# Kernel tuning notes

Hardware: AMD Instinct MI355X
Metric: run time of the kernel (lower is better)

The kernel has to match this reference:

```python
import jax, jax.numpy as jnp
import numpy as np

S = 3136        # tokens (56x56 patch grid, single image segment -> full attention)
H = 16          # num_heads
D = 80          # head_dim (= head_dim_ori = PADDING_HEAD_DIM)
HID = H * D     # 1280
SCALE = 1.0 / float(np.sqrt(D))  # qkScale = 1/sqrt(head_dim_ori)


def _rope_tables(s, d, base=10000.0):
    # rotate_half style: cos/sin of shape [s, d], duplicated over the two halves
    half = d // 2
    inv_freq = 1.0 / (base ** (np.arange(0, half, dtype=np.float32) / half))
    freqs = np.outer(np.arange(s, dtype=np.float32), inv_freq)  # [s, d/2]
    emb = np.concatenate([freqs, freqs], axis=-1)               # [s, d]
    return jnp.asarray(np.cos(emb)), jnp.asarray(np.sin(emb))


def setup_inputs() -> dict:
    key = jax.random.key(0)
    ks = jax.random.split(key, 6)
    cos, sin = _rope_tables(S, D)
    return {
        "hidden_states": jax.random.normal(ks[0], (S, HID), jnp.float32),
        "x_norm": jax.random.normal(ks[1], (S, HID), jnp.float32),
        "qkv_w": jax.random.normal(ks[2], (3 * HID, HID), jnp.float32) * 0.02,
        "qkv_b": jax.random.normal(ks[3], (3 * HID,), jnp.float32) * 0.02,
        "proj_w": jax.random.normal(ks[4], (HID, HID), jnp.float32) * 0.02,
        "proj_b": jax.random.normal(ks[5], (HID,), jnp.float32) * 0.02,
        "cos": cos,
        "sin": sin,
    }


def _rotate_half(x):
    x1, x2 = jnp.split(x, 2, axis=-1)
    return jnp.concatenate([-x2, x1], axis=-1)


def reference(hidden_states, x_norm, qkv_w, qkv_b, proj_w, proj_b, cos, sin):
    # fused QKV linear (transposeB=True) + split into q,k,v along last dim
    qkv = x_norm @ qkv_w.T + qkv_b                      # [S, 3*HID]
    q, k, v = jnp.split(qkv, 3, axis=-1)                # each [S, HID]
    q = q.reshape(S, H, D)
    k = k.reshape(S, H, D)
    v = v.reshape(S, H, D)
    # inline RoPE on q and k (rotate_half over full head_dim)
    c = cos[:, None, :]; s = sin[:, None, :]           # [S,1,D]
    q = q * c + _rotate_half(q) * s
    k = k * c + _rotate_half(k) * s
    # full self-attention (PA_ENCODER, single segment = seq_len S)
    scores = jnp.einsum('shd,thd->hst', q, k) * SCALE   # [H,S,S]
    probs = jax.nn.softmax(scores, axis=-1)
    attn = jnp.einsum('hst,thd->shd', probs, v)         # [S,H,D]
    attn = attn.reshape(S, HID)
    # output projection + residual add
    out = attn @ proj_w.T + proj_b
    return hidden_states + out
```

## Files before the change

kernel.cpp:

```cpp
#include <hip/hip_runtime.h>
#include <hip/hip_bf16.h>

#define S_   3136
#define H_   16
#define D_   80
#define DP_  96
#define HID_ 1280

typedef short  bf16x8 __attribute__((ext_vector_type(8)));
typedef short  bf16x4 __attribute__((ext_vector_type(4)));
typedef float  f32x4  __attribute__((ext_vector_type(4)));

__device__ __forceinline__ float b2f(unsigned short u) {
    union { unsigned int i; float f; } c;
    c.i = ((unsigned int)u) << 16;
    return c.f;
}
__device__ __forceinline__ unsigned short f2b(float f) {
    union { unsigned int i; float f; } c;
    c.f = f;
    unsigned int x = c.i;
    unsigned int lsb = (x >> 16) & 1u;
    x += 0x7fffu + lsb;
    return (unsigned short)(x >> 16);
}
__device__ __forceinline__ unsigned int cvt_pk_bf16(float lo, float hi) {
    unsigned int r;
    asm("v_cvt_pk_bf16_f32 %0, %1, %2" : "=v"(r) : "v"(lo), "v"(hi));
    return r;
}

#define N4_X 1003520
#define N4_Q 1228800
#define N4_P 409600

__global__ __launch_bounds__(256)
void cast3_kernel(const float* __restrict__ x0, unsigned short* __restrict__ y0,
                  const float* __restrict__ x1, unsigned short* __restrict__ y1,
                  const float* __restrict__ x2, unsigned short* __restrict__ y2)
{
    int i = blockIdx.x * 256 + threadIdx.x;
    const float* src; unsigned short* dst;
    if (i < N4_X)               { src = x0; dst = y0; }
    else if (i < N4_X + N4_Q)   { src = x1; dst = y1; i -= N4_X; }
    else if (i < N4_X + N4_Q + N4_P) { src = x2; dst = y2; i -= N4_X + N4_Q; }
    else return;
    float4 v = ((const float4*)src)[i];
    ushort4 o;
    o.x = f2b(v.x); o.y = f2b(v.y); o.z = f2b(v.z); o.w = f2b(v.w);
    ((ushort4*)dst)[i] = o;
}

#define ASTR 40

__global__ __launch_bounds__(256)
void qkv_mfma_kernel(const unsigned short* __restrict__ Ab,
                     const unsigned short* __restrict__ Wb,
                     const float* __restrict__ bias,
                     unsigned short* __restrict__ qo, unsigned short* __restrict__ ko,
                     unsigned short* __restrict__ vtb)
{
    __shared__ __align__(16) short As[2][128][ASTR];
    __shared__ __align__(16) short Bs[2][128][ASTR];
    int m0 = blockIdx.x * 128;
    int n0 = blockIdx.y * 128;
    int t = threadIdx.x;
    int wave = t >> 6, lane = t & 63, lq = lane & 15, quad = lane >> 4;
    int wr = wave >> 1, wc = wave & 1;

    int r0  = t >> 2;
    int r1  = r0 + 64;
    int kc0 = (t & 3) << 3;
    const unsigned short* pa0 = Ab + (size_t)min(m0 + r0, S_ - 1) * HID_ + kc0;
    const unsigned short* pa1 = Ab + (size_t)min(m0 + r1, S_ - 1) * HID_ + kc0;
    const unsigned short* pb0 = Wb + (size_t)(n0 + r0) * HID_ + kc0;
    const unsigned short* pb1 = Wb + (size_t)(n0 + r1) * HID_ + kc0;

    const bf16x8* afp[2][4]; const bf16x8* bfp[2][4];
    #pragma unroll
    for (int s = 0; s < 2; ++s)
        #pragma unroll
        for (int i = 0; i < 4; ++i) {
            afp[s][i] = (const bf16x8*)&As[s][wr * 64 + i * 16 + lq][quad * 8];
            bfp[s][i] = (const bf16x8*)&Bs[s][wc * 64 + i * 16 + lq][quad * 8];
        }

    f32x4 acc[4][4];
    #pragma unroll
    for (int i = 0; i < 4; ++i)
        #pragma unroll
        for (int j = 0; j < 4; ++j) acc[i][j] = (f32x4){0.f, 0.f, 0.f, 0.f};

    bf16x8 va[2][2], vb[2][2];
    #pragma unroll
    for (int s = 0; s < 2; ++s) {
        va[s][0] = *(const bf16x8*)(pa0 + s * 32);
        va[s][1] = *(const bf16x8*)(pa1 + s * 32);
        vb[s][0] = *(const bf16x8*)(pb0 + s * 32);
        vb[s][1] = *(const bf16x8*)(pb1 + s * 32);
    }

    for (int kt = 0; kt < HID_; kt += 64) {
        __syncthreads();
        #pragma unroll
        for (int s = 0; s < 2; ++s) {
            *(bf16x8*)&As[s][r0][kc0] = va[s][0];
            *(bf16x8*)&As[s][r1][kc0] = va[s][1];
            *(bf16x8*)&Bs[s][r0][kc0] = vb[s][0];
            *(bf16x8*)&Bs[s][r1][kc0] = vb[s][1];
        }
        __syncthreads();
        if (kt + 64 < HID_) {
            #pragma unroll
            for (int s = 0; s < 2; ++s) {
                va[s][0] = *(const bf16x8*)(pa0 + kt + 64 + s * 32);
                va[s][1] = *(const bf16x8*)(pa1 + kt + 64 + s * 32);
                vb[s][0] = *(const bf16x8*)(pb0 + kt + 64 + s * 32);
                vb[s][1] = *(const bf16x8*)(pb1 + kt + 64 + s * 32);
            }
        }
        #pragma unroll
        for (int s = 0; s < 2; ++s) {
            bf16x8 af[4], bfr[4];
            #pragma unroll
            for (int i = 0; i < 4; ++i) af[i]  = *afp[s][i];
            #pragma unroll
            for (int j = 0; j < 4; ++j) bfr[j] = *bfp[s][j];
            #pragma unroll
            for (int i = 0; i < 4; ++i)
                #pragma unroll
                for (int j = 0; j < 4; ++j)
                    acc[i][j] = __builtin_amdgcn_mfma_f32_16x16x32_bf16(af[i], bfr[j], acc[i][j], 0, 0, 0);
        }
    }

    #pragma unroll
    for (int i = 0; i < 4; ++i)
        #pragma unroll
        for (int j = 0; j < 4; ++j)
            #pragma unroll
            for (int reg = 0; reg < 4; ++reg) {
                int row = m0 + wr * 64 + i * 16 + quad * 4 + reg;
                if (row >= S_) continue;
                int col = n0 + wc * 64 + j * 16 + lq;
                float val = acc[i][j][reg] + bias[col];
                int which = col / HID_;
                int rem   = col - which * HID_;
                int h     = rem / D_;
                int d     = rem - h * D_;
                if (which == 0)      qo[((size_t)h * S_ + row) * D_ + d] = f2b(val);
                else if (which == 1) ko[((size_t)h * S_ + row) * D_ + d] = f2b(val);
                else                 vtb[((size_t)h * D_ + d) * S_ + row] = f2b(val);
            }
}

__global__ __launch_bounds__(256)
void proj_mfma_kernel(const unsigned short* __restrict__ Ab,
                      const unsigned short* __restrict__ Wb,
                      const float* __restrict__ bias, const float* __restrict__ hidden,
                      float* __restrict__ out)
{
    __shared__ __align__(16) short As[64][ASTR];
    __shared__ __align__(16) short Bs[64][ASTR];
    int m0 = blockIdx.x * 64;
    int n0 = blockIdx.y * 64;
    int t = threadIdx.x;
    int wave = t >> 6, lane = t & 63, lq = lane & 15, quad = lane >> 4;
    int wr = wave >> 1, wc = wave & 1;

    int r  = t >> 2;
    int kc0 = (t & 3) << 3;
    const unsigned short* pa = Ab + (size_t)(m0 + r) * HID_ + kc0;
    const unsigned short* pb = Wb + (size_t)(n0 + r) * HID_ + kc0;
    short* sa = &As[r][kc0];
    short* sb = &Bs[r][kc0];

    const bf16x8* afp[2]; const bf16x8* bfp[2];
    #pragma unroll
    for (int i = 0; i < 2; ++i) {
        afp[i] = (const bf16x8*)&As[wr * 32 + i * 16 + lq][quad * 8];
        bfp[i] = (const bf16x8*)&Bs[wc * 32 + i * 16 + lq][quad * 8];
    }

    f32x4 acc[2][2];
    #pragma unroll
    for (int i = 0; i < 2; ++i)
        #pragma unroll
        for (int j = 0; j < 2; ++j) acc[i][j] = (f32x4){0.f, 0.f, 0.f, 0.f};

    bf16x8 va = *(const bf16x8*)(pa);
    bf16x8 vb = *(const bf16x8*)(pb);

    for (int kt = 0; kt < HID_; kt += 32) {
        __syncthreads();
        *(bf16x8*)sa = va;
        *(bf16x8*)sb = vb;
        __syncthreads();
        if (kt + 32 < HID_) {
            va = *(const bf16x8*)(pa + kt + 32);
            vb = *(const bf16x8*)(pb + kt + 32);
        }
        bf16x8 af[2], bfr[2];
        #pragma unroll
        for (int i = 0; i < 2; ++i) af[i]  = *afp[i];
        #pragma unroll
        for (int j = 0; j < 2; ++j) bfr[j] = *bfp[j];
        #pragma unroll
        for (int i = 0; i < 2; ++i)
            #pragma unroll
            for (int j = 0; j < 2; ++j)
                acc[i][j] = __builtin_amdgcn_mfma_f32_16x16x32_bf16(af[i], bfr[j], acc[i][j], 0, 0, 0);
    }

    #pragma unroll
    for (int i = 0; i < 2; ++i)
        #pragma unroll
        for (int j = 0; j < 2; ++j)
            #pragma unroll
            for (int reg = 0; reg < 4; ++reg) {
                int row = m0 + wr * 32 + i * 16 + quad * 4 + reg;
                int col = n0 + wc * 32 + j * 16 + lq;
                out[(size_t)row * HID_ + col] =
                    acc[i][j][reg] + bias[col] + hidden[(size_t)row * HID_ + col];
            }
}

__global__ void rope_kernel(const unsigned short* __restrict__ q, const unsigned short* __restrict__ k,
                            const float* __restrict__ cost, const float* __restrict__ sint,
                            unsigned short* __restrict__ qb, unsigned short* __restrict__ kb)
{
    const float QSCALE = 0.11180339887498949f * 1.4426950408889634f;
    int idx = blockIdx.x * 256 + threadIdx.x;
    const int total = H_ * S_ * 40;
    if (idx >= total) return;
    int d  = idx % 40;
    int hs = idx / 40;
    int s  = hs % S_;
    size_t base  = (size_t)hs * D_;
    size_t base9 = (size_t)hs * DP_;
    float c1 = cost[s * D_ + d];
    float s1 = sint[s * D_ + d];
    float c2 = cost[s * D_ + d + 40];
    float s2 = sint[s * D_ + d + 40];
    float x1 = b2f(q[base + d]), x2 = b2f(q[base + d + 40]);
    qb[base9 + d]      = f2b((x1 * c1 - x2 * s1) * QSCALE);
    qb[base9 + d + 40] = f2b((x2 * c2 + x1 * s2) * QSCALE);
    x1 = b2f(k[base + d]); x2 = b2f(k[base + d + 40]);
    kb[base9 + d]      = f2b(x1 * c1 - x2 * s1);
    kb[base9 + d + 40] = f2b(x2 * c2 + x1 * s2);
    if (d < 16) {
        qb[base9 + 80 + d] = 0;
        kb[base9 + 80 + d] = 0;
    }
}

#define KSTRIDE 104
#define VSTRIDE 72

__global__ __launch_bounds__(256)
void attn_kernel(const unsigned short* __restrict__ Qb,
                 const unsigned short* __restrict__ Kb,
                 const unsigned short* __restrict__ Vtb,
                 unsigned short* __restrict__ attnb)
{
    __shared__ __align__(16) short Ks[64][KSTRIDE];
    __shared__ __align__(16) short Vs[80][VSTRIDE];

    int h   = blockIdx.y;
    int qb0 = blockIdx.x * 64;
    int t    = threadIdx.x;
    int wave = t >> 6;
    int lane = t & 63;
    int lq   = lane & 15;
    int quad = lane >> 4;

    const unsigned short* Qrow = Qb + ((size_t)h * S_ + qb0 + wave * 16 + lq) * DP_;
    bf16x8 qf[3];
    #pragma unroll
    for (int kc = 0; kc < 3; ++kc)
        qf[kc] = *(const bf16x8*)(Qrow + kc * 32 + quad * 8);

    f32x4 O[5];
    #pragma unroll
    for (int dt = 0; dt < 5; ++dt) O[dt] = (f32x4){0.f, 0.f, 0.f, 0.f};
    float l_acc = 0.f;

    int srow = t & 63;
    int w    = t >> 6;
    int vr0  = t >> 3;
    int vc   = (t & 7) << 3;
    const unsigned short* Kg = Kb  + (size_t)h * S_ * DP_ + (size_t)srow * DP_;
    const unsigned short* Vg = Vtb + (size_t)h * D_ * S_;
    short* kl0 = &Ks[srow][(w    ) * 8];
    short* kl1 = &Ks[srow][(w + 4) * 8];
    short* kl2 = &Ks[srow][(w + 8) * 8];

    const int NKB = S_ / 64;
    bf16x8 pk0, pk1, pk2, pv0, pv1, pv2;
    {
        pk0 = *(const bf16x8*)(Kg + (w    ) * 8);
        pk1 = *(const bf16x8*)(Kg + (w + 4) * 8);
        pk2 = *(const bf16x8*)(Kg + (w + 8) * 8);
        const unsigned short* vg = Vg + vc;
        pv0 = *(const bf16x8*)(vg + (size_t)(vr0     ) * S_);
        pv1 = *(const bf16x8*)(vg + (size_t)(vr0 + 32) * S_);
        if (vr0 < 16) pv2 = *(const bf16x8*)(vg + (size_t)(vr0 + 64) * S_);
    }

    for (int kb = 0; kb < NKB; ++kb) {
        __syncthreads();
        *(bf16x8*)kl0 = pk0;
        *(bf16x8*)kl1 = pk1;
        *(bf16x8*)kl2 = pk2;
        *(bf16x8*)&Vs[vr0     ][vc] = pv0;
        *(bf16x8*)&Vs[vr0 + 32][vc] = pv1;
        if (vr0 < 16) *(bf16x8*)&Vs[vr0 + 64][vc] = pv2;
        __syncthreads();

        if (kb + 1 < NKB) {
            const unsigned short* kg = Kg + (size_t)(kb + 1) * 64 * DP_;
            pk0 = *(const bf16x8*)(kg + (w    ) * 8);
            pk1 = *(const bf16x8*)(kg + (w + 4) * 8);
            pk2 = *(const bf16x8*)(kg + (w + 8) * 8);
            const unsigned short* vg = Vg + (kb + 1) * 64 + vc;
            pv0 = *(const bf16x8*)(vg + (size_t)(vr0     ) * S_);
            pv1 = *(const bf16x8*)(vg + (size_t)(vr0 + 32) * S_);
            if (vr0 < 16) pv2 = *(const bf16x8*)(vg + (size_t)(vr0 + 64) * S_);
        }

        f32x4 sc[4];
        #pragma unroll
        for (int nt = 0; nt < 4; ++nt) {
            sc[nt] = (f32x4){0.f, 0.f, 0.f, 0.f};
            #pragma unroll
            for (int kc = 0; kc < 3; ++kc) {
                bf16x8 kf = *(const bf16x8*)&Ks[nt * 16 + lq][kc * 32 + quad * 8];
                sc[nt] = __builtin_amdgcn_mfma_f32_16x16x32_bf16(kf, qf[kc], sc[nt], 0, 0, 0);
            }
        }

        float p[4][4];
        #pragma unroll
        for (int nt = 0; nt < 4; ++nt)
            #pragma unroll
            for (int r = 0; r < 4; ++r)
                p[nt][r] = exp2f(sc[nt][r]);

        l_acc += ((p[0][0] + p[0][1]) + (p[0][2] + p[0][3]))
               + ((p[1][0] + p[1][1]) + (p[1][2] + p[1][3]))
               + ((p[2][0] + p[2][1]) + (p[2][2] + p[2][3]))
               + ((p[3][0] + p[3][1]) + (p[3][2] + p[3][3]));

        union { bf16x8 v8; unsigned int d[4]; } pa[2];
        #pragma unroll
        for (int kc = 0; kc < 2; ++kc) {
            pa[kc].d[0] = cvt_pk_bf16(p[2 * kc    ][0], p[2 * kc    ][1]);
            pa[kc].d[1] = cvt_pk_bf16(p[2 * kc    ][2], p[2 * kc    ][3]);
            pa[kc].d[2] = cvt_pk_bf16(p[2 * kc + 1][0], p[2 * kc + 1][1]);
            pa[kc].d[3] = cvt_pk_bf16(p[2 * kc + 1][2], p[2 * kc + 1][3]);
        }

        #pragma unroll
        for (int kc = 0; kc < 2; ++kc) {
            #pragma unroll
            for (int dt = 0; dt < 5; ++dt) {
                union { bf16x8 v8; bf16x4 v4[2]; } vv;
                vv.v4[0] = *(const bf16x4*)&Vs[dt * 16 + lq][kc * 32 +      quad * 4];
                vv.v4[1] = *(const bf16x4*)&Vs[dt * 16 + lq][kc * 32 + 16 + quad * 4];
                O[dt] = __builtin_amdgcn_mfma_f32_16x16x32_bf16(pa[kc].v8, vv.v8, O[dt], 0, 0, 0);
            }
        }
    }

    float lf = l_acc;
    lf += __shfl_xor(lf, 16);
    lf += __shfl_xor(lf, 32);
    #pragma unroll
    for (int reg = 0; reg < 4; ++reg) {
        float l = __shfl(lf, quad * 4 + reg, 16);
        float linv = 1.0f / l;
        int s = qb0 + wave * 16 + quad * 4 + reg;
        unsigned short* orow = attnb + (size_t)s * HID_ + h * D_;
        #pragma unroll
        for (int dt = 0; dt < 5; ++dt)
            orow[dt * 16 + lq] = f2b(O[dt][reg] * linv);
    }
}

extern "C" void kernel_launch(void* const* d_in, const int* in_sizes, int n_in,
                              void* d_out, int out_size, void* d_ws, size_t ws_size,
                              hipStream_t stream)
{
    const float* hidden = (const float*)d_in[0];
    const float* x_norm = (const float*)d_in[1];
    const float* qkv_w  = (const float*)d_in[2];
    const float* qkv_b  = (const float*)d_in[3];
    const float* proj_w = (const float*)d_in[4];
    const float* proj_b = (const float*)d_in[5];
    const float* cost   = (const float*)d_in[6];
    const float* sint   = (const float*)d_in[7];
    float* out = (float*)d_out;

    unsigned short* w      = (unsigned short*)d_ws;
    unsigned short* qbuf   = w;
    unsigned short* kbuf   = qbuf + 4014080;
    unsigned short* vtb    = kbuf + 4014080;
    unsigned short* kbb    = vtb + 4064256;
    unsigned short* xb     = kbb + 4816896;
    unsigned short* wqkvb  = xb + 4014080;
    unsigned short* wprojb = wqkvb + 4915200;
    unsigned short* qbb    = wqkvb;
    unsigned short* abuf   = qbuf;

    cast3_kernel<<<(N4_X + N4_Q + N4_P + 255) / 256, 256, 0, stream>>>(
        x_norm, xb, qkv_w, wqkvb, proj_w, wprojb);

    qkv_mfma_kernel<<<dim3(25, 30), 256, 0, stream>>>(xb, wqkvb, qkv_b, qbuf, kbuf, vtb);
    rope_kernel<<<(H_ * S_ * 40 + 255) / 256, 256, 0, stream>>>(qbuf, kbuf, cost, sint, qbb, kbb);
    attn_kernel<<<dim3(S_ / 64, H_), 256, 0, stream>>>(qbb, kbb, vtb, abuf);
    proj_mfma_kernel<<<dim3(49, 20), 256, 0, stream>>>(abuf, wprojb, proj_b, hidden, out);
}
```

Before: 338.2 us.

## Restructure attention kernel with key-stripe split, direct-to-LDS loads, and swizzled LDS

The attention kernel now has each wave handle 32 query rows over one of two interleaved 64-key stripes, so every K/V fragment read from LDS feeds two MFMAs. The two stripes' partial outputs and row sums are combined through shared memory at the end. K and V tiles are loaded with global_load_lds straight into an XOR-swizzled LDS layout, replacing the register-staged copy and the padded strides. The register prefetch double-buffering is dropped: each iteration waits on vmcnt(0) and a barrier before compute, which risks exposing load latency, and LDS use grows to 52KB, which may reduce occupancy.

```diff
diff --git a/kernel.cpp b/kernel.cpp
--- a/kernel.cpp
+++ b/kernel.cpp
@@ -28,6 +28,12 @@
     unsigned int r;
     asm("v_cvt_pk_bf16_f32 %0, %1, %2" : "=v"(r) : "v"(lo), "v"(hi));
     return r;
+}
+
+typedef const void __attribute__((address_space(1))) GAS;
+typedef void __attribute__((address_space(3))) LAS;
+__device__ __forceinline__ void gl16(const void* g, void* l) {
+    __builtin_amdgcn_global_load_lds((GAS*)g, (LAS*)l, 16, 0, 0);
 }
 
 #define N4_X 1003520
@@ -254,136 +260,163 @@
     }
 }
 
-#define KSTRIDE 104
-#define VSTRIDE 72
-
 __global__ __launch_bounds__(256)
 void attn_kernel(const unsigned short* __restrict__ Qb,
                  const unsigned short* __restrict__ Kb,
                  const unsigned short* __restrict__ Vtb,
                  unsigned short* __restrict__ attnb)
 {
-    __shared__ __align__(16) short Ks[64][KSTRIDE];
-    __shared__ __align__(16) short Vs[80][VSTRIDE];
+    __shared__ __align__(16) unsigned char smem[53248];
 
     int h   = blockIdx.y;
     int qb0 = blockIdx.x * 64;
-    int t    = threadIdx.x;
-    int wave = t >> 6;
-    int lane = t & 63;
-    int lq   = lane & 15;
-    int quad = lane >> 4;
-
-    const unsigned short* Qrow = Qb + ((size_t)h * S_ + qb0 + wave * 16 + lq) * DP_;
-    bf16x8 qf[3];
-    #pragma unroll
-    for (int kc = 0; kc < 3; ++kc)
-        qf[kc] = *(const bf16x8*)(Qrow + kc * 32 + quad * 8);
-
-    f32x4 O[5];
-    #pragma unroll
-    for (int dt = 0; dt < 5; ++dt) O[dt] = (f32x4){0.f, 0.f, 0.f, 0.f};
-    float l_acc = 0.f;
-
-    int srow = t & 63;
-    int w    = t >> 6;
-    int vr0  = t >> 3;
-    int vc   = (t & 7) << 3;
-    const unsigned short* Kg = Kb  + (size_t)h * S_ * DP_ + (size_t)srow * DP_;
-    const unsigned short* Vg = Vtb + (size_t)h * D_ * S_;
-    short* kl0 = &Ks[srow][(w    ) * 8];
-    short* kl1 = &Ks[srow][(w + 4) * 8];
-    short* kl2 = &Ks[srow][(w + 8) * 8];
-
-    const int NKB = S_ / 64;
-    bf16x8 pk0, pk1, pk2, pv0, pv1, pv2;
-    {
-        pk0 = *(const bf16x8*)(Kg + (w    ) * 8);
-        pk1 = *(const bf16x8*)(Kg + (w + 4) * 8);
-        pk2 = *(const bf16x8*)(Kg + (w + 8) * 8);
-        const unsigned short* vg = Vg + vc;
-        pv0 = *(const bf16x8*)(vg + (size_t)(vr0     ) * S_);
-        pv1 = *(const bf16x8*)(vg + (size_t)(vr0 + 32) * S_);
-        if (vr0 < 16) pv2 = *(const bf16x8*)(vg + (size_t)(vr0 + 64) * S_);
-    }
-
-    for (int kb = 0; kb < NKB; ++kb) {
-        __syncthreads();
-        *(bf16x8*)kl0 = pk0;
-        *(bf16x8*)kl1 = pk1;
-        *(bf16x8*)kl2 = pk2;
-        *(bf16x8*)&Vs[vr0     ][vc] = pv0;
-        *(bf16x8*)&Vs[vr0 + 32][vc] = pv1;
-        if (vr0 < 16) *(bf16x8*)&Vs[vr0 + 64][vc] = pv2;
-        __syncthreads();
-
-        if (kb + 1 < NKB) {
-            const unsigned short* kg = Kg + (size_t)(kb + 1) * 64 * DP_;
-            pk0 = *(const bf16x8*)(kg + (w    ) * 8);
-            pk1 = *(const bf16x8*)(kg + (w + 4) * 8);
-            pk2 = *(const bf16x8*)(kg + (w + 8) * 8);
-            const unsigned short* vg = Vg + (kb + 1) * 64 + vc;
-            pv0 = *(const bf16x8*)(vg + (size_t)(vr0     ) * S_);
-            pv1 = *(const bf16x8*)(vg + (size_t)(vr0 + 32) * S_);
-            if (vr0 < 16) pv2 = *(const bf16x8*)(vg + (size_t)(vr0 + 64) * S_);
-        }
-
-        f32x4 sc[4];
-        #pragma unroll
-        for (int nt = 0; nt < 4; ++nt) {
-            sc[nt] = (f32x4){0.f, 0.f, 0.f, 0.f};
-            #pragma unroll
-            for (int kc = 0; kc < 3; ++kc) {
-                bf16x8 kf = *(const bf16x8*)&Ks[nt * 16 + lq][kc * 32 + quad * 8];
-                sc[nt] = __builtin_amdgcn_mfma_f32_16x16x32_bf16(kf, qf[kc], sc[nt], 0, 0, 0);
-            }
-        }
-
-        float p[4][4];
-        #pragma unroll
-        for (int nt = 0; nt < 4; ++nt)
-            #pragma unroll
-            for (int r = 0; r < 4; ++r)
-                p[nt][r] = exp2f(sc[nt][r]);
-
-        l_acc += ((p[0][0] + p[0][1]) + (p[0][2] + p[0][3]))
-               + ((p[1][0] + p[1][1]) + (p[1][2] + p[1][3]))
-               + ((p[2][0] + p[2][1]) + (p[2][2] + p[2][3]))
-               + ((p[3][0] + p[3][1]) + (p[3][2] + p[3][3]));
-
-        union { bf16x8 v8; unsigned int d[4]; } pa[2];
-        #pragma unroll
-        for (int kc = 0; kc < 2; ++kc) {
-            pa[kc].d[0] = cvt_pk_bf16(p[2 * kc    ][0], p[2 * kc    ][1]);
-            pa[kc].d[1] = cvt_pk_bf16(p[2 * kc    ][2], p[2 * kc    ][3]);
-            pa[kc].d[2] = cvt_pk_bf16(p[2 * kc + 1][0], p[2 * kc + 1][1]);
-            pa[kc].d[3] = cvt_pk_bf16(p[2 * kc + 1][2], p[2 * kc + 1][3]);
-        }
-
-        #pragma unroll
-        for (int kc = 0; kc < 2; ++kc) {
-            #pragma unroll
-            for (int dt = 0; dt < 5; ++dt) {
-                union { bf16x8 v8; bf16x4 v4[2]; } vv;
-                vv.v4[0] = *(const bf16x4*)&Vs[dt * 16 + lq][kc * 32 +      quad * 4];
-                vv.v4[1] = *(const bf16x4*)&Vs[dt * 16 + lq][kc * 32 + 16 + quad * 4];
-                O[dt] = __builtin_amdgcn_mfma_f32_16x16x32_bf16(pa[kc].v8, vv.v8, O[dt], 0, 0, 0);
-            }
-        }
-    }
-
-    float lf = l_acc;
-    lf += __shfl_xor(lf, 16);
-    lf += __shfl_xor(lf, 32);
-    #pragma unroll
-    for (int reg = 0; reg < 4; ++reg) {
-        float l = __shfl(lf, quad * 4 + reg, 16);
-        float linv = 1.0f / l;
-        int s = qb0 + wave * 16 + quad * 4 + reg;
-        unsigned short* orow = attnb + (size_t)s * HID_ + h * D_;
-        #pragma unroll
-        for (int dt = 0; dt < 5; ++dt)
-            orow[dt * 16 + lq] = f2b(O[dt][reg] * linv);
+    int t      = threadIdx.x;
+    int wave   = t >> 6;
+    int lane   = t & 63;
+    int lq     = lane & 15;
+    int quad   = lane >> 4;
+    int qh     = wave & 1;
+    int stripe = wave >> 1;
+    int Q0     = qb0 + qh * 32;
+    int swz    = (lq & 7) << 4;
+
+    bf16x8 qf[2][3];
+    #pragma unroll
+    for (int qt = 0; qt < 2; ++qt)
+        #pragma unroll
+        for (int kc = 0; kc < 3; ++kc)
+            qf[qt][kc] = *(const bf16x8*)(Qb + ((size_t)h * S_ + Q0 + qt * 16 + lq) * DP_ + kc * 32 + quad * 8);
+
+    f32x4 O[2][5];
+    #pragma unroll
+    for (int qt = 0; qt < 2; ++qt)
+        #pragma unroll
+        for (int dt = 0; dt < 5; ++dt) O[qt][dt] = (f32x4){0.f, 0.f, 0.f, 0.f};
+    float l_acc[2] = {0.f, 0.f};
+
+    const int NR = (S_ + 127) / 128;
+
+    for (int r = 0; r < NR; ++r) {
+        int kbase = r * 128;
+        bool stv = (kbase + stripe * 64) < S_;
+
+        if (stv) {
+            #pragma unroll
+            for (int ii = 0; ii < 8; ++ii) {
+                int i  = wave * 8 + ii;
+                int rb = (i & 15) * 4;
+                int rl = rb + (lane >> 4);
+                int kg = kbase + stripe * 64 + rl;
+                const unsigned short* src = Kb + ((size_t)h * S_ + kg) * DP_
+                                          + (((((lane & 15) * 16) ^ ((rl & 7) << 4))) >> 1);
+                gl16(src, smem + stripe * 16384 + rb * 256);
+            }
+            #pragma unroll
+            for (int jj = 0; jj < 5; ++jj) {
+                int j  = wave * 5 + jj;
+                int jl = j - stripe * 10;
+                int db = jl * 8;
+                int d  = db + (lane >> 3);
+                int scol = kbase + stripe * 64 + (((((lane & 7) * 16) ^ ((d & 7) << 4))) >> 1);
+                gl16(Vtb + (size_t)(h * D_ + d) * S_ + scol,
+                     smem + 32768 + stripe * 10240 + db * 128);
+            }
+        }
+        asm volatile("s_waitcnt vmcnt(0)" ::: "memory");
+        __syncthreads();
+
+        if (stv) {
+            union PaU { bf16x8 v8; unsigned int d[4]; };
+            PaU pa[2][2];
+
+            #pragma unroll
+            for (int kcp = 0; kcp < 2; ++kcp) {
+                f32x4 sc[2][2];
+                #pragma unroll
+                for (int sub = 0; sub < 2; ++sub) {
+                    int kt = kcp * 2 + sub;
+                    const unsigned char* kb = smem + stripe * 16384 + (kt * 16 + lq) * 256;
+                    bf16x8 kf0 = *(const bf16x8*)(kb + (((0 * 64 + quad * 16)) ^ swz));
+                    bf16x8 kf1 = *(const bf16x8*)(kb + (((1 * 64 + quad * 16)) ^ swz));
+                    bf16x8 kf2 = *(const bf16x8*)(kb + (((2 * 64 + quad * 16)) ^ swz));
+                    #pragma unroll
+                    for (int qt = 0; qt < 2; ++qt) {
+                        f32x4 a = (f32x4){0.f, 0.f, 0.f, 0.f};
+                        a = __builtin_amdgcn_mfma_f32_16x16x32_bf16(kf0, qf[qt][0], a, 0, 0, 0);
+                        a = __builtin_amdgcn_mfma_f32_16x16x32_bf16(kf1, qf[qt][1], a, 0, 0, 0);
+                        a = __builtin_amdgcn_mfma_f32_16x16x32_bf16(kf2, qf[qt][2], a, 0, 0, 0);
+                        sc[qt][sub] = a;
+                    }
+                }
+                #pragma unroll
+                for (int qt = 0; qt < 2; ++qt) {
+                    float e00 = exp2f(sc[qt][0][0]), e01 = exp2f(sc[qt][0][1]);
+                    float e02 = exp2f(sc[qt][0][2]), e03 = exp2f(sc[qt][0][3]);
+                    float e10 = exp2f(sc[qt][1][0]), e11 = exp2f(sc[qt][1][1]);
+                    float e12 = exp2f(sc[qt][1][2]), e13 = exp2f(sc[qt][1][3]);
+                    l_acc[qt] += ((e00 + e01) + (e02 + e03)) + ((e10 + e11) + (e12 + e13));
+                    pa[qt][kcp].d[0] = cvt_pk_bf16(e00, e01);
+                    pa[qt][kcp].d[1] = cvt_pk_bf16(e02, e03);
+                    pa[qt][kcp].d[2] = cvt_pk_bf16(e10, e11);
+                    pa[qt][kcp].d[3] = cvt_pk_bf16(e12, e13);
+                }
+            }
+
+            #pragma unroll
+            for (int kcp = 0; kcp < 2; ++kcp) {
+                #pragma unroll
+                for (int dt = 0; dt < 5; ++dt) {
+                    const unsigned char* vb = smem + 32768 + stripe * 10240 + (dt * 16 + lq) * 128;
+                    union { bf16x8 v8; bf16x4 v4[2]; } vv;
+                    vv.v4[0] = *(const bf16x4*)(vb + (((kcp * 64 + quad * 8)) ^ swz));
+                    vv.v4[1] = *(const bf16x4*)(vb + (((kcp * 64 + 32 + quad * 8)) ^ swz));
+                    #pragma unroll
+                    for (int qt = 0; qt < 2; ++qt)
+                        O[qt][dt] = __builtin_amdgcn_mfma_f32_16x16x32_bf16(pa[qt][kcp].v8, vv.v8, O[qt][dt], 0, 0, 0);
+                }
+            }
+        }
+        __syncthreads();
+    }
+
+    float lr[2];
+    #pragma unroll
+    for (int qt = 0; qt < 2; ++qt) {
+        float l = l_acc[qt];
+        l += __shfl_xor(l, 16);
+        l += __shfl_xor(l, 32);
+        lr[qt] = l;
+    }
+    f32x4* Of = (f32x4*)smem;
+    float* Lf = (float*)(smem + 20480);
+    if (stripe == 1) {
+        #pragma unroll
+        for (int qt = 0; qt < 2; ++qt) {
+            #pragma unroll
+            for (int dt = 0; dt < 5; ++dt)
+                Of[((qh * 2 + qt) * 5 + dt) * 64 + lane] = O[qt][dt];
+            if (lane < 16) Lf[(qh * 2 + qt) * 16 + lane] = lr[qt];
+        }
+    }
+    __syncthreads();
+    if (stripe == 0) {
+        #pragma unroll
+        for (int qt = 0; qt < 2; ++qt) {
+            float ltot = lr[qt] + Lf[(qh * 2 + qt) * 16 + lq];
+            #pragma unroll
+            for (int dt = 0; dt < 5; ++dt)
+                O[qt][dt] += Of[((qh * 2 + qt) * 5 + dt) * 64 + lane];
+            #pragma unroll
+            for (int reg = 0; reg < 4; ++reg) {
+                float l = __shfl(ltot, quad * 4 + reg, 16);
+                float linv = 1.0f / l;
+                int s = Q0 + qt * 16 + quad * 4 + reg;
+                unsigned short* orow = attnb + (size_t)s * HID_ + h * D_;
+                #pragma unroll
+                for (int dt = 0; dt < 5; ++dt)
+                    orow[dt * 16 + lq] = f2b(O[qt][dt][reg] * linv);
+            }
+        }
     }
 }
 
```

Result: faster. 326.5 us (-3.5%).
